# Optimization experiments

Hardware: AMD Instinct MI355X
Metric: run time of the kernel (lower is better)

Reference implementation:

```python
import jax, jax.numpy as jnp
import numpy as np

B, S, D, H = 2, 2048, 1024, 16
DH = D // H  # 64


def setup_inputs() -> dict:
    key = jax.random.key(0)
    ks = jax.random.split(key, 12)
    scale = 0.02
    q = jax.random.normal(ks[0], (B, S, D), dtype=jnp.float32)
    k = jax.random.normal(ks[1], (B, S, D), dtype=jnp.float32)
    v = jax.random.normal(ks[2], (B, S, D), dtype=jnp.float32)
    # CTRL-style causal mask: 1.0 above the diagonal (positions to mask), 0.0 elsewhere
    mask = jnp.triu(jnp.ones((S, S), dtype=jnp.float32), k=1)
    Wq = jax.random.normal(ks[3], (D, D), dtype=jnp.float32) * scale
    bq = jnp.zeros((D,), dtype=jnp.float32)
    Wk = jax.random.normal(ks[4], (D, D), dtype=jnp.float32) * scale
    bk = jnp.zeros((D,), dtype=jnp.float32)
    Wv = jax.random.normal(ks[5], (D, D), dtype=jnp.float32) * scale
    bv = jnp.zeros((D,), dtype=jnp.float32)
    Wo = jax.random.normal(ks[6], (D, D), dtype=jnp.float32) * scale
    bo = jnp.zeros((D,), dtype=jnp.float32)
    return {"q": q, "k": k, "v": v, "mask": mask,
            "Wq": Wq, "bq": bq, "Wk": Wk, "bk": bk,
            "Wv": Wv, "bv": bv, "Wo": Wo, "bo": bo}


def _split_heads(x):
    # [B, S, D] -> [B, H, S, DH]
    b, s, _ = x.shape
    return x.reshape(b, s, H, DH).transpose(0, 2, 1, 3)


def reference(q, k, v, mask, Wq, bq, Wk, bk, Wv, bv, Wo, bo):
    # QKV projections
    qh = _split_heads(q @ Wq + bq)  # [B, H, S, DH]
    kh = _split_heads(k @ Wk + bk)
    vh = _split_heads(v @ Wv + bv)
    # scaled dot-product attention with CTRL mask convention (mask * -1e4 added)
    scores = jnp.einsum('bhqd,bhkd->bhqk', qh, kh) / jnp.sqrt(jnp.float32(DH))
    scores = scores + mask * -10000.0  # mask broadcasts [S,S] -> [B,H,S,S]
    weights = jax.nn.softmax(scores, axis=-1)
    ctx = jnp.einsum('bhqk,bhkd->bhqd', weights, vh)  # [B, H, S, DH]
    ctx = ctx.transpose(0, 2, 1, 3).reshape(q.shape[0], -1, D)  # [B, S, D]
    return ctx @ Wo + bo
```

## Files before the change

kernel.cpp:

```cpp
#include <hip/hip_runtime.h>
#include <stdint.h>

typedef unsigned short u16;
typedef __attribute__((ext_vector_type(8))) short bf16x8;
typedef __attribute__((ext_vector_type(4))) float f32x4;
typedef __attribute__((ext_vector_type(4))) unsigned short u16x4;

#define C_SCALE 0.1803368801111204f
#define C_MASK  -14426.950408889634f

__device__ __forceinline__ float bf2f(u16 x) {
  union { uint32_t u; float f; } v; v.u = ((uint32_t)x) << 16; return v.f;
}
__device__ __forceinline__ u16 f2bf(float f) {
  union { float f; uint32_t u; } v; v.f = f;
  return (u16)((v.u + 0x7FFFu + ((v.u >> 16) & 1u)) >> 16);
}

__device__ __forceinline__ void load_lds16(const void* g, void* l) {
  __builtin_amdgcn_global_load_lds(
      (const __attribute__((address_space(1))) uint32_t*)g,
      (__attribute__((address_space(3))) uint32_t*)l, 16, 0, 0);
}

__device__ __forceinline__ uint32_t pack_trunc(uint32_t f_even, uint32_t f_odd) {
  return __builtin_amdgcn_perm(f_odd, f_even, 0x07060302u);
}

__device__ __forceinline__ bool detect_bf16(const u16* __restrict__ q) {
  int lane = threadIdx.x & 63;
  u16 w = q[lane * 4];
  int e = (w >> 7) & 0xFF;
  unsigned long long b = __ballot(e >= 96 && e <= 159);
  return __popcll(b) >= 48;
}

__global__ __launch_bounds__(256) void transpose_all(const u16* __restrict__ W0,
                                                     const u16* __restrict__ W1,
                                                     const u16* __restrict__ W2,
                                                     const u16* __restrict__ W3,
                                                     u16* __restrict__ WTb,
                                                     const u16* __restrict__ qprobe) {
  constexpr int D = 1024;
  __shared__ u16 tile[64][72];
  const int z = blockIdx.z;
  const u16* W = z == 0 ? W0 : (z == 1 ? W1 : (z == 2 ? W2 : W3));
  u16* WT = WTb + (size_t)z * D * D;
  const bool isbf = detect_bf16(qprobe);
  const int x0 = blockIdx.x * 64, y0 = blockIdx.y * 64;
  const int t = threadIdx.x;
  const int r = t >> 3;
  const int c8 = (t & 7) << 3;
#pragma unroll
  for (int hh = 0; hh < 2; ++hh) {
    int row = r + hh * 32;
    if (isbf) {
      *(uint4*)&tile[row][c8] = *(const uint4*)&W[(size_t)(y0 + row) * D + x0 + c8];
    } else {
      const float* Wf = (const float*)W;
      float4 f0 = *(const float4*)&Wf[(size_t)(y0 + row) * D + x0 + c8];
      float4 f1 = *(const float4*)&Wf[(size_t)(y0 + row) * D + x0 + c8 + 4];
      u16 tmp[8] = {f2bf(f0.x), f2bf(f0.y), f2bf(f0.z), f2bf(f0.w),
                    f2bf(f1.x), f2bf(f1.y), f2bf(f1.z), f2bf(f1.w)};
      *(uint4*)&tile[row][c8] = *(uint4*)tmp;
    }
  }
  __syncthreads();
#pragma unroll
  for (int hh = 0; hh < 2; ++hh) {
    int row = r + hh * 32;
    u16 tmp[8];
#pragma unroll
    for (int i = 0; i < 8; ++i) tmp[i] = tile[c8 + i][row];
    *(uint4*)&WT[(size_t)(x0 + row) * D + y0 + c8] = *(uint4*)tmp;
  }
}

__global__ __launch_bounds__(256, 2) void gemm_qkv(
    const u16* __restrict__ A0, const u16* __restrict__ A1, const u16* __restrict__ A2,
    const u16* __restrict__ WTb,
    const u16* __restrict__ b0, const u16* __restrict__ b1, const u16* __restrict__ b2,
    u16* __restrict__ Chb) {
  constexpr int K = 1024;
  __shared__ u16 As[2][64 * 32];
  __shared__ u16 Bs[2][128 * 32];
  const int z = blockIdx.z;
  const u16* A = z == 0 ? A0 : (z == 1 ? A1 : A2);
  const u16* bias = z == 0 ? b0 : (z == 1 ? b1 : b2);
  const u16* BT = WTb + (size_t)z * 1024 * 1024;
  u16* C = Chb + (size_t)z * 4 * 1024 * 1024;
  const bool isbf = detect_bf16(A0);
  const int tid = threadIdx.x;
  const int wave = tid >> 6, lane = tid & 63;
  const int quad = lane >> 4, lr = lane & 15;
  const int f = blockIdx.x + 8 * blockIdx.y;
  const int n0 = (f >> 6) * 128;
  const int m0 = (f & 63) * 64;
  const int mW = (wave & 1) * 32, nW = (wave >> 1) * 64;
  const int ar = tid >> 2, ac = (tid & 3) * 8;

  uint4 ra, rb;
  auto loadA = [&](int k0) {
    if (isbf) {
      ra = *(const uint4*)&A[(size_t)(m0 + ar) * K + k0 + ac];
    } else {
      const uint32_t* Af = (const uint32_t*)A;
      ra = *(const uint4*)&Af[(size_t)(m0 + ar) * K + k0 + ac];
      rb = *(const uint4*)&Af[(size_t)(m0 + ar) * K + k0 + ac + 4];
    }
  };
  auto writeA = [&](int kb) {
    if (isbf) {
      *(uint4*)&As[kb][ar * 32 + ac] = ra;
    } else {
      uint4 o;
      o.x = pack_trunc(ra.x, ra.y); o.y = pack_trunc(ra.z, ra.w);
      o.z = pack_trunc(rb.x, rb.y); o.w = pack_trunc(rb.z, rb.w);
      *(uint4*)&As[kb][ar * 32 + ac] = o;
    }
  };
  auto stageB = [&](int k0, int kb) {
#pragma unroll
    for (int p = 0; p < 2; ++p) {
      int s = (wave * 2 + p) * 64 + lane;
      int r = s >> 2, c = s & 3;
      load_lds16(&BT[(size_t)(n0 + r) * K + k0 + c * 8], &Bs[kb][(wave * 2 + p) * 512]);
    }
  };

  f32x4 acc[2][4] = {};
  loadA(0);
  stageB(0, 0);
  writeA(0);
  loadA(32);
  int kb = 0;
  for (int k0 = 0; k0 < K; k0 += 32, kb ^= 1) {
    __syncthreads();
    if (k0 + 32 < K) {
      stageB(k0 + 32, kb ^ 1);
      writeA(kb ^ 1);
      if (k0 + 64 < K) loadA(k0 + 64);
    }
    bf16x8 af[2], bfm[4];
#pragma unroll
    for (int i = 0; i < 2; ++i)
      af[i] = *(const bf16x8*)&As[kb][(mW + 16 * i + lr) * 32 + quad * 8];
#pragma unroll
    for (int j = 0; j < 4; ++j)
      bfm[j] = *(const bf16x8*)&Bs[kb][(nW + 16 * j + lr) * 32 + quad * 8];
#pragma unroll
    for (int i = 0; i < 2; ++i)
#pragma unroll
      for (int j = 0; j < 4; ++j)
        acc[i][j] =
            __builtin_amdgcn_mfma_f32_16x16x32_bf16(af[i], bfm[j], acc[i][j], 0, 0, 0);
  }

#pragma unroll
  for (int i = 0; i < 2; ++i) {
#pragma unroll
    for (int j = 0; j < 4; ++j) {
      int n = n0 + nW + 16 * j + lr;
      float bv = isbf ? bf2f(bias[n]) : ((const float*)bias)[n];
#pragma unroll
      for (int r = 0; r < 4; ++r) {
        int m = m0 + mW + 16 * i + quad * 4 + r;
        float val = acc[i][j][r] + bv;
        int b = m >> 11, s = m & 2047, h = n >> 6, dh = n & 63;
        C[((size_t)(b * 16 + h) * 2048 + s) * 64 + dh] = f2bf(val);
      }
    }
  }
}

__global__ __launch_bounds__(256, 2) void gemm_out(const u16* __restrict__ A,
                                                   const u16* __restrict__ BT,
                                                   const u16* __restrict__ bias,
                                                   u16* __restrict__ C,
                                                   const u16* __restrict__ qprobe) {
  constexpr int K = 1024, N = 1024;
  __shared__ u16 As[2][64 * 32];
  __shared__ u16 Bs[2][64 * 32];
  const bool isbf = detect_bf16(qprobe);
  const int tid = threadIdx.x;
  const int wave = tid >> 6, lane = tid & 63;
  const int quad = lane >> 4, lr = lane & 15;
  const int f = blockIdx.x + 8 * blockIdx.y;
  const int n0 = (f >> 6) * 64;
  const int m0 = (f & 63) * 64;
  const int mW = (wave & 1) * 32, nW = (wave >> 1) * 32;

  auto stage = [&](int k0, int kb) {
    int s = wave * 64 + lane;
    int r = s >> 2, c = s & 3;
    load_lds16(&A[(size_t)(m0 + r) * K + k0 + c * 8], &As[kb][wave * 512]);
    load_lds16(&BT[(size_t)(n0 + r) * K + k0 + c * 8], &Bs[kb][wave * 512]);
  };

  f32x4 acc[2][2] = {};
  stage(0, 0);
  int kb = 0;
  for (int k0 = 0; k0 < K; k0 += 32, kb ^= 1) {
    __syncthreads();
    if (k0 + 32 < K) stage(k0 + 32, kb ^ 1);
    bf16x8 af[2], bfm[2];
#pragma unroll
    for (int i = 0; i < 2; ++i) {
      af[i]  = *(const bf16x8*)&As[kb][(mW + 16 * i + lr) * 32 + quad * 8];
      bfm[i] = *(const bf16x8*)&Bs[kb][(nW + 16 * i + lr) * 32 + quad * 8];
    }
#pragma unroll
    for (int i = 0; i < 2; ++i)
#pragma unroll
      for (int j = 0; j < 2; ++j)
        acc[i][j] =
            __builtin_amdgcn_mfma_f32_16x16x32_bf16(af[i], bfm[j], acc[i][j], 0, 0, 0);
  }

#pragma unroll
  for (int i = 0; i < 2; ++i) {
#pragma unroll
    for (int j = 0; j < 2; ++j) {
      int n = n0 + nW + 16 * j + lr;
      float bv = isbf ? bf2f(bias[n]) : ((const float*)bias)[n];
#pragma unroll
      for (int r = 0; r < 4; ++r) {
        int m = m0 + mW + 16 * i + quad * 4 + r;
        float val = acc[i][j][r] + bv;
        size_t idx = (size_t)m * N + n;
        if (isbf) C[idx] = f2bf(val);
        else ((float*)C)[idx] = val;
      }
    }
  }
}

__global__ __launch_bounds__(256, 2) void attn_fwd(const u16* __restrict__ Qh,
                                                   const u16* __restrict__ Kh,
                                                   const u16* __restrict__ Vh,
                                                   u16* __restrict__ ctx) {
  constexpr int S = 2048, DH = 64, Dm = 1024;
  __shared__ u16 Ks[2][64 * 64];
  __shared__ u16 Vt[2][64 * 72];
  __shared__ u16 Pl[4][16 * 72];
  const int tid = threadIdx.x;
  const int wave = tid >> 6, lane = tid & 63;
  const int quad = lane >> 4, lr = lane & 15;
  const int bh = blockIdx.y;
  const int bx = (int)blockIdx.x;
  const size_t base = (size_t)bh * S * DH;
  const u16* Q = Qh + base;
  const u16* Kp = Kh + base;
  const u16* Vp = Vh + base;
  u16* Plw = Pl[wave];
  const int b = bh >> 4, h = bh & 15;

  const int vkey2 = (tid & 31) * 2, vd8 = (tid >> 5) * 8;
  uint4 va, vbr;

  auto stageK = [&](int kt, int kbuf) {
#pragma unroll
    for (int p = 0; p < 2; ++p) {
      int s = (wave * 2 + p) * 64 + lane;
      int r = s >> 3, cg = (s & 7) ^ (r & 7);
      load_lds16(&Kp[(size_t)(kt + r) * DH + cg * 8], &Ks[kbuf][(wave * 2 + p) * 512]);
    }
  };
  auto loadV = [&](int kt) {
    va  = *(const uint4*)&Vp[(size_t)(kt + vkey2) * DH + vd8];
    vbr = *(const uint4*)&Vp[(size_t)(kt + vkey2 + 1) * DH + vd8];
  };
  auto writeV = [&](int vbuf) {
    const u16* pa = (const u16*)&va;
    const u16* pb = (const u16*)&vbr;
#pragma unroll
    for (int i = 0; i < 8; ++i) {
      uint32_t pair = (uint32_t)pa[i] | ((uint32_t)pb[i] << 16);
      *(uint32_t*)&Vt[vbuf][(vd8 + i) * 72 + vkey2] = pair;
    }
  };

  int kb = 0, vb = 0;
  for (int ph = 0; ph < 2; ++ph) {
    const int qt = ph == 0 ? (31 - bx) : bx;
    const int q0 = qt * 64;
    const int nt = qt + 1;
    const int qg = q0 + wave * 16 + lr;

    bf16x8 aQ[2];
#pragma unroll
    for (int s = 0; s < 2; ++s)
      aQ[s] = *(const bf16x8*)&Q[(size_t)(q0 + wave * 16 + lr) * DH + s * 32 + quad * 8];

    f32x4 o[4] = {};
    float m_i = -1.0e5f;
    float l_i = 0.f;

    __syncthreads();
    stageK(0, kb);
    loadV(0);
    writeV(vb);
    if (nt > 1) loadV(64);

    for (int it = 0; it < nt; ++it) {
      const int kt = it * 64;
      __syncthreads();

      bf16x8 aK[4][2], bV[4][2];
#pragma unroll
      for (int t = 0; t < 4; ++t) {
        int r = t * 16 + lr;
#pragma unroll
        for (int s = 0; s < 2; ++s) {
          int ch = (s * 4 + quad) ^ (r & 7);
          aK[t][s] = *(const bf16x8*)&Ks[kb][r * 64 + ch * 8];
        }
      }
#pragma unroll
      for (int c = 0; c < 4; ++c)
#pragma unroll
        for (int s = 0; s < 2; ++s)
          bV[c][s] = *(const bf16x8*)&Vt[vb][(c * 16 + lr) * 72 + s * 32 + quad * 8];

      if (it + 1 < nt) {
        stageK(kt + 64, kb ^ 1);
        writeV(vb ^ 1);
        if (it + 2 < nt) loadV(kt + 128);
      }

      f32x4 sc[4];
#pragma unroll
      for (int t = 0; t < 4; ++t) {
        f32x4 zz = {0.f, 0.f, 0.f, 0.f};
        zz = __builtin_amdgcn_mfma_f32_16x16x32_bf16(aK[t][0], aQ[0], zz, 0, 0, 0);
        zz = __builtin_amdgcn_mfma_f32_16x16x32_bf16(aK[t][1], aQ[1], zz, 0, 0, 0);
        sc[t] = zz;
      }

      const bool diag = (it == nt - 1);
      float v[4][4];
      float mx = -1.0e5f;
      if (diag) {
#pragma unroll
        for (int t = 0; t < 4; ++t)
#pragma unroll
          for (int r = 0; r < 4; ++r) {
            int kg = kt + t * 16 + quad * 4 + r;
            float x = sc[t][r] * C_SCALE + ((kg > qg) ? C_MASK : 0.f);
            v[t][r] = x;
            mx = fmaxf(mx, x);
          }
      } else {
#pragma unroll
        for (int t = 0; t < 4; ++t)
#pragma unroll
          for (int r = 0; r < 4; ++r) {
            float x = sc[t][r] * C_SCALE;
            v[t][r] = x;
            mx = fmaxf(mx, x);
          }
      }
      mx = fmaxf(mx, __shfl_xor(mx, 16));
      mx = fmaxf(mx, __shfl_xor(mx, 32));
      float m_new = fmaxf(m_i, mx);
      float sum = 0.f;
      u16 pb16[4][4];
#pragma unroll
      for (int t = 0; t < 4; ++t)
#pragma unroll
        for (int r = 0; r < 4; ++r) {
          float p = exp2f(v[t][r] - m_new);
          sum += p;
          pb16[t][r] = f2bf(p);
        }
      sum += __shfl_xor(sum, 16);
      sum += __shfl_xor(sum, 32);
      float alpha = exp2f(m_i - m_new);
      l_i = l_i * alpha + sum;
      m_i = m_new;
#pragma unroll
      for (int t = 0; t < 4; ++t) {
        u16x4 w = {pb16[t][0], pb16[t][1], pb16[t][2], pb16[t][3]};
        *(u16x4*)&Plw[lr * 72 + t * 16 + quad * 4] = w;
      }
#pragma unroll
      for (int r = 0; r < 4; ++r) {
        float ab = __shfl(alpha, quad * 4 + r);
#pragma unroll
        for (int c = 0; c < 4; ++c) o[c][r] *= ab;
      }
      asm volatile("s_waitcnt lgkmcnt(0)" ::: "memory");
      bf16x8 aP[2];
#pragma unroll
      for (int s = 0; s < 2; ++s)
        aP[s] = *(const bf16x8*)&Plw[lr * 72 + s * 32 + quad * 8];
#pragma unroll
      for (int c = 0; c < 4; ++c)
#pragma unroll
        for (int s = 0; s < 2; ++s)
          o[c] = __builtin_amdgcn_mfma_f32_16x16x32_bf16(aP[s], bV[c][s], o[c], 0, 0, 0);
      kb ^= 1; vb ^= 1;
    }

    float linv = 1.f / l_i;
#pragma unroll
    for (int r = 0; r < 4; ++r) {
      float lb = __shfl(linv, quad * 4 + r);
      int s = q0 + wave * 16 + quad * 4 + r;
      size_t orow = ((size_t)b * S + s) * Dm + h * DH;
#pragma unroll
      for (int c = 0; c < 4; ++c) ctx[orow + c * 16 + lr] = f2bf(o[c][r] * lb);
    }
  }
}

extern "C" void kernel_launch(void* const* d_in, const int* in_sizes, int n_in,
                              void* d_out, int out_size, void* d_ws, size_t ws_size,
                              hipStream_t stream) {
  const u16* q  = (const u16*)d_in[0];
  const u16* k  = (const u16*)d_in[1];
  const u16* v  = (const u16*)d_in[2];
  const u16* Wq = (const u16*)d_in[4];
  const u16* bq = (const u16*)d_in[5];
  const u16* Wk = (const u16*)d_in[6];
  const u16* bk = (const u16*)d_in[7];
  const u16* Wv = (const u16*)d_in[8];
  const u16* bv = (const u16*)d_in[9];
  const u16* Wo = (const u16*)d_in[10];
  const u16* bo = (const u16*)d_in[11];
  u16* out = (u16*)d_out;

  constexpr size_t M1 = 1024 * 1024;
  u16* ws = (u16*)d_ws;
  u16* WT  = ws;
  u16* Qh  = WT + 4 * M1;
  u16* ctx = Qh + 12 * M1;

  dim3 tb(256);
  transpose_all<<<dim3(16, 16, 4), tb, 0, stream>>>(Wq, Wk, Wv, Wo, WT, q);
  gemm_qkv<<<dim3(8, 64, 3), tb, 0, stream>>>(q, k, v, WT, bq, bk, bv, Qh);
  attn_fwd<<<dim3(16, 32), tb, 0, stream>>>(Qh, Qh + 4 * M1, Qh + 8 * M1, ctx);
  gemm_out<<<dim3(8, 128), tb, 0, stream>>>(ctx, WT + 3 * M1, bo, out, q);
}
```

Baseline: 262.2 us.

## Deepen GEMM pipelines to four LDS stages with XOR swizzle and wider out tiles

Both projection GEMMs move from double-buffered to four-stage LDS buffering and process two K-tiles per barrier, which halves the number of __syncthreads and gives loads more lead time. B tiles (and the out-GEMM's A tiles) are stored with an XOR column swizzle, and the QKV A tile gets a padded row stride of 40, both aimed at LDS bank conflicts. The output GEMM tile grows from 64x64 to 64x128 with half as many blocks. More LDS per block may reduce occupancy, and the smaller out-GEMM grid may underfill the GPU.

```diff
diff --git a/kernel.cpp b/kernel.cpp
--- a/kernel.cpp
+++ b/kernel.cpp
@@ -82,8 +82,8 @@
     const u16* __restrict__ b0, const u16* __restrict__ b1, const u16* __restrict__ b2,
     u16* __restrict__ Chb) {
   constexpr int K = 1024;
-  __shared__ u16 As[2][64 * 32];
-  __shared__ u16 Bs[2][128 * 32];
+  __shared__ u16 As[4][64 * 40];
+  __shared__ u16 Bs[4][128 * 32];
   const int z = blockIdx.z;
   const u16* A = z == 0 ? A0 : (z == 1 ? A1 : A2);
   const u16* bias = z == 0 ? b0 : (z == 1 ? b1 : b2);
@@ -97,75 +97,91 @@
   const int n0 = (f >> 6) * 128;
   const int m0 = (f & 63) * 64;
   const int mW = (wave & 1) * 32, nW = (wave >> 1) * 64;
-  const int ar = tid >> 2, ac = (tid & 3) * 8;
-
-  uint4 ra, rb;
-  auto loadA = [&](int k0) {
+  const int ar = tid >> 2, ac = tid & 3;
+
+  uint4 ra[2][2];
+  auto loadA = [&](int t) {
+    int slot = t & 1, k0 = t * 32;
     if (isbf) {
-      ra = *(const uint4*)&A[(size_t)(m0 + ar) * K + k0 + ac];
+      ra[slot][0] = *(const uint4*)&A[(size_t)(m0 + ar) * K + k0 + ac * 8];
     } else {
       const uint32_t* Af = (const uint32_t*)A;
-      ra = *(const uint4*)&Af[(size_t)(m0 + ar) * K + k0 + ac];
-      rb = *(const uint4*)&Af[(size_t)(m0 + ar) * K + k0 + ac + 4];
-    }
-  };
-  auto writeA = [&](int kb) {
+      ra[slot][0] = *(const uint4*)&Af[(size_t)(m0 + ar) * K + k0 + ac * 8];
+      ra[slot][1] = *(const uint4*)&Af[(size_t)(m0 + ar) * K + k0 + ac * 8 + 4];
+    }
+  };
+  auto writeA = [&](int t) {
+    int slot = t & 1, buf = t & 3;
     if (isbf) {
-      *(uint4*)&As[kb][ar * 32 + ac] = ra;
+      *(uint4*)&As[buf][ar * 40 + ac * 8] = ra[slot][0];
     } else {
       uint4 o;
-      o.x = pack_trunc(ra.x, ra.y); o.y = pack_trunc(ra.z, ra.w);
-      o.z = pack_trunc(rb.x, rb.y); o.w = pack_trunc(rb.z, rb.w);
-      *(uint4*)&As[kb][ar * 32 + ac] = o;
-    }
-  };
-  auto stageB = [&](int k0, int kb) {
+      o.x = pack_trunc(ra[slot][0].x, ra[slot][0].y);
+      o.y = pack_trunc(ra[slot][0].z, ra[slot][0].w);
+      o.z = pack_trunc(ra[slot][1].x, ra[slot][1].y);
+      o.w = pack_trunc(ra[slot][1].z, ra[slot][1].w);
+      *(uint4*)&As[buf][ar * 40 + ac * 8] = o;
+    }
+  };
+  auto stageB = [&](int t) {
+    int buf = t & 3, k0 = t * 32;
 #pragma unroll
     for (int p = 0; p < 2; ++p) {
       int s = (wave * 2 + p) * 64 + lane;
       int r = s >> 2, c = s & 3;
-      load_lds16(&BT[(size_t)(n0 + r) * K + k0 + c * 8], &Bs[kb][(wave * 2 + p) * 512]);
+      int cg = c ^ (r & 3);
+      load_lds16(&BT[(size_t)(n0 + r) * K + k0 + cg * 8],
+                 &Bs[buf][(wave * 2 + p) * 512]);
     }
   };
 
   f32x4 acc[2][4] = {};
-  loadA(0);
-  stageB(0, 0);
-  writeA(0);
-  loadA(32);
-  int kb = 0;
-  for (int k0 = 0; k0 < K; k0 += 32, kb ^= 1) {
+
+  loadA(0); loadA(1);
+  stageB(0); stageB(1);
+  writeA(0); writeA(1);
+  loadA(2); loadA(3);
+  __syncthreads();
+
+  for (int j = 0; j < 16; ++j) {
+    const int tc0 = 2 * j, tc1 = 2 * j + 1;
+    if (tc0 + 2 < 32) {
+      writeA(tc0 + 2); writeA(tc1 + 2);
+      stageB(tc0 + 2); stageB(tc1 + 2);
+      if (tc0 + 4 < 32) { loadA(tc0 + 4); loadA(tc1 + 4); }
+    }
+#pragma unroll
+    for (int tt = 0; tt < 2; ++tt) {
+      const int buf = (tc0 + tt) & 3;
+      bf16x8 af[2], bfm[4];
+#pragma unroll
+      for (int i = 0; i < 2; ++i)
+        af[i] = *(const bf16x8*)&As[buf][(mW + 16 * i + lr) * 40 + quad * 8];
+#pragma unroll
+      for (int jj = 0; jj < 4; ++jj) {
+        int rr = nW + 16 * jj + lr;
+        bfm[jj] = *(const bf16x8*)&Bs[buf][rr * 32 + ((quad ^ (rr & 3)) * 8)];
+      }
+#pragma unroll
+      for (int i = 0; i < 2; ++i)
+#pragma unroll
+        for (int jj = 0; jj < 4; ++jj)
+          acc[i][jj] =
+              __builtin_amdgcn_mfma_f32_16x16x32_bf16(af[i], bfm[jj], acc[i][jj], 0, 0, 0);
+    }
     __syncthreads();
-    if (k0 + 32 < K) {
-      stageB(k0 + 32, kb ^ 1);
-      writeA(kb ^ 1);
-      if (k0 + 64 < K) loadA(k0 + 64);
-    }
-    bf16x8 af[2], bfm[4];
-#pragma unroll
-    for (int i = 0; i < 2; ++i)
-      af[i] = *(const bf16x8*)&As[kb][(mW + 16 * i + lr) * 32 + quad * 8];
-#pragma unroll
-    for (int j = 0; j < 4; ++j)
-      bfm[j] = *(const bf16x8*)&Bs[kb][(nW + 16 * j + lr) * 32 + quad * 8];
-#pragma unroll
-    for (int i = 0; i < 2; ++i)
-#pragma unroll
-      for (int j = 0; j < 4; ++j)
-        acc[i][j] =
-            __builtin_amdgcn_mfma_f32_16x16x32_bf16(af[i], bfm[j], acc[i][j], 0, 0, 0);
   }
 
 #pragma unroll
   for (int i = 0; i < 2; ++i) {
 #pragma unroll
-    for (int j = 0; j < 4; ++j) {
-      int n = n0 + nW + 16 * j + lr;
+    for (int jj = 0; jj < 4; ++jj) {
+      int n = n0 + nW + 16 * jj + lr;
       float bv = isbf ? bf2f(bias[n]) : ((const float*)bias)[n];
 #pragma unroll
       for (int r = 0; r < 4; ++r) {
         int m = m0 + mW + 16 * i + quad * 4 + r;
-        float val = acc[i][j][r] + bv;
+        float val = acc[i][jj][r] + bv;
         int b = m >> 11, s = m & 2047, h = n >> 6, dh = n & 63;
         C[((size_t)(b * 16 + h) * 2048 + s) * 64 + dh] = f2bf(val);
       }
@@ -179,54 +195,76 @@
                                                    u16* __restrict__ C,
                                                    const u16* __restrict__ qprobe) {
   constexpr int K = 1024, N = 1024;
-  __shared__ u16 As[2][64 * 32];
-  __shared__ u16 Bs[2][64 * 32];
+  __shared__ u16 As[4][64 * 32];
+  __shared__ u16 Bs[4][128 * 32];
   const bool isbf = detect_bf16(qprobe);
   const int tid = threadIdx.x;
   const int wave = tid >> 6, lane = tid & 63;
   const int quad = lane >> 4, lr = lane & 15;
   const int f = blockIdx.x + 8 * blockIdx.y;
-  const int n0 = (f >> 6) * 64;
+  const int n0 = (f >> 6) * 128;
   const int m0 = (f & 63) * 64;
-  const int mW = (wave & 1) * 32, nW = (wave >> 1) * 32;
-
-  auto stage = [&](int k0, int kb) {
-    int s = wave * 64 + lane;
-    int r = s >> 2, c = s & 3;
-    load_lds16(&A[(size_t)(m0 + r) * K + k0 + c * 8], &As[kb][wave * 512]);
-    load_lds16(&BT[(size_t)(n0 + r) * K + k0 + c * 8], &Bs[kb][wave * 512]);
-  };
-
-  f32x4 acc[2][2] = {};
-  stage(0, 0);
-  int kb = 0;
-  for (int k0 = 0; k0 < K; k0 += 32, kb ^= 1) {
+  const int mW = (wave & 1) * 32, nW = (wave >> 1) * 64;
+
+  auto stage = [&](int t) {
+    int buf = t & 3, k0 = t * 32;
+    {
+      int s = wave * 64 + lane;
+      int r = s >> 2, c = s & 3;
+      int cg = c ^ (r & 3);
+      load_lds16(&A[(size_t)(m0 + r) * K + k0 + cg * 8], &As[buf][wave * 512]);
+    }
+#pragma unroll
+    for (int p = 0; p < 2; ++p) {
+      int s = (wave * 2 + p) * 64 + lane;
+      int r = s >> 2, c = s & 3;
+      int cg = c ^ (r & 3);
+      load_lds16(&BT[(size_t)(n0 + r) * K + k0 + cg * 8],
+                 &Bs[buf][(wave * 2 + p) * 512]);
+    }
+  };
+
+  f32x4 acc[2][4] = {};
+  stage(0); stage(1);
+  __syncthreads();
+
+  for (int j = 0; j < 16; ++j) {
+    const int tc0 = 2 * j;
+    if (tc0 + 2 < 32) { stage(tc0 + 2); stage(tc0 + 3); }
+#pragma unroll
+    for (int tt = 0; tt < 2; ++tt) {
+      const int buf = (tc0 + tt) & 3;
+      bf16x8 af[2], bfm[4];
+#pragma unroll
+      for (int i = 0; i < 2; ++i) {
+        int rr = mW + 16 * i + lr;
+        af[i] = *(const bf16x8*)&As[buf][rr * 32 + ((quad ^ (rr & 3)) * 8)];
+      }
+#pragma unroll
+      for (int jj = 0; jj < 4; ++jj) {
+        int rr = nW + 16 * jj + lr;
+        bfm[jj] = *(const bf16x8*)&Bs[buf][rr * 32 + ((quad ^ (rr & 3)) * 8)];
+      }
+#pragma unroll
+      for (int i = 0; i < 2; ++i)
+#pragma unroll
+        for (int jj = 0; jj < 4; ++jj)
+          acc[i][jj] =
+              __builtin_amdgcn_mfma_f32_16x16x32_bf16(af[i], bfm[jj], acc[i][jj], 0, 0, 0);
+    }
     __syncthreads();
-    if (k0 + 32 < K) stage(k0 + 32, kb ^ 1);
-    bf16x8 af[2], bfm[2];
-#pragma unroll
-    for (int i = 0; i < 2; ++i) {
-      af[i]  = *(const bf16x8*)&As[kb][(mW + 16 * i + lr) * 32 + quad * 8];
-      bfm[i] = *(const bf16x8*)&Bs[kb][(nW + 16 * i + lr) * 32 + quad * 8];
-    }
-#pragma unroll
-    for (int i = 0; i < 2; ++i)
-#pragma unroll
-      for (int j = 0; j < 2; ++j)
-        acc[i][j] =
-            __builtin_amdgcn_mfma_f32_16x16x32_bf16(af[i], bfm[j], acc[i][j], 0, 0, 0);
   }
 
 #pragma unroll
   for (int i = 0; i < 2; ++i) {
 #pragma unroll
-    for (int j = 0; j < 2; ++j) {
-      int n = n0 + nW + 16 * j + lr;
+    for (int jj = 0; jj < 4; ++jj) {
+      int n = n0 + nW + 16 * jj + lr;
       float bv = isbf ? bf2f(bias[n]) : ((const float*)bias)[n];
 #pragma unroll
       for (int r = 0; r < 4; ++r) {
         int m = m0 + mW + 16 * i + quad * 4 + r;
-        float val = acc[i][j][r] + bv;
+        float val = acc[i][jj][r] + bv;
         size_t idx = (size_t)m * N + n;
         if (isbf) C[idx] = f2bf(val);
         else ((float*)C)[idx] = val;
@@ -440,5 +478,5 @@
   transpose_all<<<dim3(16, 16, 4), tb, 0, stream>>>(Wq, Wk, Wv, Wo, WT, q);
   gemm_qkv<<<dim3(8, 64, 3), tb, 0, stream>>>(q, k, v, WT, bq, bk, bv, Qh);
   attn_fwd<<<dim3(16, 32), tb, 0, stream>>>(Qh, Qh + 4 * M1, Qh + 8 * M1, ctx);
-  gemm_out<<<dim3(8, 128), tb, 0, stream>>>(ctx, WT + 3 * M1, bo, out, q);
-}
+  gemm_out<<<dim3(8, 64), tb, 0, stream>>>(ctx, WT + 3 * M1, bo, out, q);
+}
```

New measurement: 252.4 us. -3.7%, faster.

## Drop LDS staging in projection GEMMs and load MFMA fragments directly from global

Applied to the files above, without the earlier changes.

Both projection GEMMs stop staging tiles through shared memory with double buffering and barriers. Each wave now loads its MFMA operand fragments straight from global memory, relying on cache for reuse. Tiles are enlarged (QKV to 128x128, output to 64x128) and launch bounds are raised to allow more resident blocks. This removes LDS traffic and barrier stalls, but every wave now fetches overlapping data from global memory with fragment-sized, less coalesced accesses, and nothing is prefetched ahead of use.

```diff
diff --git a/kernel.cpp b/kernel.cpp
--- a/kernel.cpp
+++ b/kernel.cpp
@@ -26,6 +26,8 @@
 __device__ __forceinline__ uint32_t pack_trunc(uint32_t f_even, uint32_t f_odd) {
   return __builtin_amdgcn_perm(f_odd, f_even, 0x07060302u);
 }
+
+union U4B { uint4 u; bf16x8 v; };
 
 __device__ __forceinline__ bool detect_bf16(const u16* __restrict__ q) {
   int lane = threadIdx.x & 63;
@@ -76,14 +78,12 @@
   }
 }
 
-__global__ __launch_bounds__(256, 2) void gemm_qkv(
+__global__ __launch_bounds__(256, 3) void gemm_qkv(
     const u16* __restrict__ A0, const u16* __restrict__ A1, const u16* __restrict__ A2,
     const u16* __restrict__ WTb,
     const u16* __restrict__ b0, const u16* __restrict__ b1, const u16* __restrict__ b2,
     u16* __restrict__ Chb) {
   constexpr int K = 1024;
-  __shared__ u16 As[2][64 * 32];
-  __shared__ u16 Bs[2][128 * 32];
   const int z = blockIdx.z;
   const u16* A = z == 0 ? A0 : (z == 1 ? A1 : A2);
   const u16* bias = z == 0 ? b0 : (z == 1 ? b1 : b2);
@@ -94,70 +94,65 @@
   const int wave = tid >> 6, lane = tid & 63;
   const int quad = lane >> 4, lr = lane & 15;
   const int f = blockIdx.x + 8 * blockIdx.y;
-  const int n0 = (f >> 6) * 128;
-  const int m0 = (f & 63) * 64;
-  const int mW = (wave & 1) * 32, nW = (wave >> 1) * 64;
-  const int ar = tid >> 2, ac = (tid & 3) * 8;
-
-  uint4 ra, rb;
-  auto loadA = [&](int k0) {
-    if (isbf) {
-      ra = *(const uint4*)&A[(size_t)(m0 + ar) * K + k0 + ac];
-    } else {
-      const uint32_t* Af = (const uint32_t*)A;
-      ra = *(const uint4*)&Af[(size_t)(m0 + ar) * K + k0 + ac];
-      rb = *(const uint4*)&Af[(size_t)(m0 + ar) * K + k0 + ac + 4];
-    }
-  };
-  auto writeA = [&](int kb) {
-    if (isbf) {
-      *(uint4*)&As[kb][ar * 32 + ac] = ra;
-    } else {
-      uint4 o;
-      o.x = pack_trunc(ra.x, ra.y); o.y = pack_trunc(ra.z, ra.w);
-      o.z = pack_trunc(rb.x, rb.y); o.w = pack_trunc(rb.z, rb.w);
-      *(uint4*)&As[kb][ar * 32 + ac] = o;
-    }
-  };
-  auto stageB = [&](int k0, int kb) {
-#pragma unroll
-    for (int p = 0; p < 2; ++p) {
-      int s = (wave * 2 + p) * 64 + lane;
-      int r = s >> 2, c = s & 3;
-      load_lds16(&BT[(size_t)(n0 + r) * K + k0 + c * 8], &Bs[kb][(wave * 2 + p) * 512]);
-    }
-  };
-
-  f32x4 acc[2][4] = {};
-  loadA(0);
-  stageB(0, 0);
-  writeA(0);
-  loadA(32);
-  int kb = 0;
-  for (int k0 = 0; k0 < K; k0 += 32, kb ^= 1) {
-    __syncthreads();
-    if (k0 + 32 < K) {
-      stageB(k0 + 32, kb ^ 1);
-      writeA(kb ^ 1);
-      if (k0 + 64 < K) loadA(k0 + 64);
-    }
-    bf16x8 af[2], bfm[4];
-#pragma unroll
-    for (int i = 0; i < 2; ++i)
-      af[i] = *(const bf16x8*)&As[kb][(mW + 16 * i + lr) * 32 + quad * 8];
-#pragma unroll
-    for (int j = 0; j < 4; ++j)
-      bfm[j] = *(const bf16x8*)&Bs[kb][(nW + 16 * j + lr) * 32 + quad * 8];
-#pragma unroll
-    for (int i = 0; i < 2; ++i)
+  const int n0 = (f >> 5) * 128;
+  const int m0 = (f & 31) * 128;
+  const int mW = (wave & 1) * 64, nW = (wave >> 1) * 64;
+
+  const u16* bp[4];
+#pragma unroll
+  for (int j = 0; j < 4; ++j) bp[j] = &BT[(size_t)(n0 + nW + 16 * j + lr) * K];
+
+  f32x4 acc[4][4] = {};
+
+  if (!isbf) {
+    const uint32_t* ap[4];
+#pragma unroll
+    for (int i = 0; i < 4; ++i)
+      ap[i] = (const uint32_t*)A + (size_t)(m0 + mW + 16 * i + lr) * K;
+#pragma unroll 2
+    for (int k0 = 0; k0 < K; k0 += 32) {
+      bf16x8 af[4], bfm[4];
+#pragma unroll
+      for (int i = 0; i < 4; ++i) {
+        uint4 lo = *(const uint4*)(ap[i] + k0 + quad * 8);
+        uint4 hi = *(const uint4*)(ap[i] + k0 + quad * 8 + 4);
+        U4B pk;
+        pk.u.x = pack_trunc(lo.x, lo.y); pk.u.y = pack_trunc(lo.z, lo.w);
+        pk.u.z = pack_trunc(hi.x, hi.y); pk.u.w = pack_trunc(hi.z, hi.w);
+        af[i] = pk.v;
+      }
 #pragma unroll
       for (int j = 0; j < 4; ++j)
-        acc[i][j] =
-            __builtin_amdgcn_mfma_f32_16x16x32_bf16(af[i], bfm[j], acc[i][j], 0, 0, 0);
-  }
-
-#pragma unroll
-  for (int i = 0; i < 2; ++i) {
+        bfm[j] = *(const bf16x8*)(bp[j] + k0 + quad * 8);
+#pragma unroll
+      for (int i = 0; i < 4; ++i)
+#pragma unroll
+        for (int j = 0; j < 4; ++j)
+          acc[i][j] =
+              __builtin_amdgcn_mfma_f32_16x16x32_bf16(af[i], bfm[j], acc[i][j], 0, 0, 0);
+    }
+  } else {
+    const u16* ap[4];
+#pragma unroll
+    for (int i = 0; i < 4; ++i) ap[i] = &A[(size_t)(m0 + mW + 16 * i + lr) * K];
+#pragma unroll 2
+    for (int k0 = 0; k0 < K; k0 += 32) {
+      bf16x8 af[4], bfm[4];
+#pragma unroll
+      for (int i = 0; i < 4; ++i) af[i] = *(const bf16x8*)(ap[i] + k0 + quad * 8);
+#pragma unroll
+      for (int j = 0; j < 4; ++j) bfm[j] = *(const bf16x8*)(bp[j] + k0 + quad * 8);
+#pragma unroll
+      for (int i = 0; i < 4; ++i)
+#pragma unroll
+        for (int j = 0; j < 4; ++j)
+          acc[i][j] =
+              __builtin_amdgcn_mfma_f32_16x16x32_bf16(af[i], bfm[j], acc[i][j], 0, 0, 0);
+    }
+  }
+
+#pragma unroll
+  for (int i = 0; i < 4; ++i) {
 #pragma unroll
     for (int j = 0; j < 4; ++j) {
       int n = n0 + nW + 16 * j + lr;
@@ -173,46 +168,40 @@
   }
 }
 
-__global__ __launch_bounds__(256, 2) void gemm_out(const u16* __restrict__ A,
+__global__ __launch_bounds__(256, 4) void gemm_out(const u16* __restrict__ A,
                                                    const u16* __restrict__ BT,
                                                    const u16* __restrict__ bias,
                                                    u16* __restrict__ C,
                                                    const u16* __restrict__ qprobe) {
   constexpr int K = 1024, N = 1024;
-  __shared__ u16 As[2][64 * 32];
-  __shared__ u16 Bs[2][64 * 32];
   const bool isbf = detect_bf16(qprobe);
   const int tid = threadIdx.x;
   const int wave = tid >> 6, lane = tid & 63;
   const int quad = lane >> 4, lr = lane & 15;
   const int f = blockIdx.x + 8 * blockIdx.y;
-  const int n0 = (f >> 6) * 64;
+  const int n0 = (f >> 6) * 128;
   const int m0 = (f & 63) * 64;
-  const int mW = (wave & 1) * 32, nW = (wave >> 1) * 32;
-
-  auto stage = [&](int k0, int kb) {
-    int s = wave * 64 + lane;
-    int r = s >> 2, c = s & 3;
-    load_lds16(&A[(size_t)(m0 + r) * K + k0 + c * 8], &As[kb][wave * 512]);
-    load_lds16(&BT[(size_t)(n0 + r) * K + k0 + c * 8], &Bs[kb][wave * 512]);
-  };
-
-  f32x4 acc[2][2] = {};
-  stage(0, 0);
-  int kb = 0;
-  for (int k0 = 0; k0 < K; k0 += 32, kb ^= 1) {
-    __syncthreads();
-    if (k0 + 32 < K) stage(k0 + 32, kb ^ 1);
-    bf16x8 af[2], bfm[2];
-#pragma unroll
-    for (int i = 0; i < 2; ++i) {
-      af[i]  = *(const bf16x8*)&As[kb][(mW + 16 * i + lr) * 32 + quad * 8];
-      bfm[i] = *(const bf16x8*)&Bs[kb][(nW + 16 * i + lr) * 32 + quad * 8];
-    }
+  const int mW = (wave & 1) * 32, nW = (wave >> 1) * 64;
+
+  const u16* ap[2];
+  const u16* bp[4];
+#pragma unroll
+  for (int i = 0; i < 2; ++i) ap[i] = &A[(size_t)(m0 + mW + 16 * i + lr) * K];
+#pragma unroll
+  for (int j = 0; j < 4; ++j) bp[j] = &BT[(size_t)(n0 + nW + 16 * j + lr) * K];
+
+  f32x4 acc[2][4] = {};
+#pragma unroll 2
+  for (int k0 = 0; k0 < K; k0 += 32) {
+    bf16x8 af[2], bfm[4];
+#pragma unroll
+    for (int i = 0; i < 2; ++i) af[i] = *(const bf16x8*)(ap[i] + k0 + quad * 8);
+#pragma unroll
+    for (int j = 0; j < 4; ++j) bfm[j] = *(const bf16x8*)(bp[j] + k0 + quad * 8);
 #pragma unroll
     for (int i = 0; i < 2; ++i)
 #pragma unroll
-      for (int j = 0; j < 2; ++j)
+      for (int j = 0; j < 4; ++j)
         acc[i][j] =
             __builtin_amdgcn_mfma_f32_16x16x32_bf16(af[i], bfm[j], acc[i][j], 0, 0, 0);
   }
@@ -220,7 +209,7 @@
 #pragma unroll
   for (int i = 0; i < 2; ++i) {
 #pragma unroll
-    for (int j = 0; j < 2; ++j) {
+    for (int j = 0; j < 4; ++j) {
       int n = n0 + nW + 16 * j + lr;
       float bv = isbf ? bf2f(bias[n]) : ((const float*)bias)[n];
 #pragma unroll
@@ -438,7 +427,7 @@
 
   dim3 tb(256);
   transpose_all<<<dim3(16, 16, 4), tb, 0, stream>>>(Wq, Wk, Wv, Wo, WT, q);
-  gemm_qkv<<<dim3(8, 64, 3), tb, 0, stream>>>(q, k, v, WT, bq, bk, bv, Qh);
+  gemm_qkv<<<dim3(8, 32, 3), tb, 0, stream>>>(q, k, v, WT, bq, bk, bv, Qh);
   attn_fwd<<<dim3(16, 32), tb, 0, stream>>>(Qh, Qh + 4 * M1, Qh + 8 * M1, ctx);
-  gemm_out<<<dim3(8, 128), tb, 0, stream>>>(ctx, WT + 3 * M1, bo, out, q);
-}
+  gemm_out<<<dim3(8, 64), tb, 0, stream>>>(ctx, WT + 3 * M1, bo, out, q);
+}
```

Result: slower. 356.5 us (+36.0%).
